# Kernel tuning notes

Hardware: AMD Instinct MI355X
Metric: run time of the kernel (lower is better)

Reference implementation:

```python
import jax, jax.numpy as jnp
import numpy as np

FACTOR = 2
GAIN = 1.0

def _setup_fir(fir=(1, 3, 3, 1), gain=GAIN):
    k = np.asarray(fir, dtype=np.float32)
    if k.ndim == 1:
        k = np.outer(k, k)
    k = k / k.sum() * gain
    return k  # (4, 4)

def setup_inputs() -> dict:
    key = jax.random.key(0)
    kx, kw = jax.random.split(key)
    N, C, H, W = 16, 320, 64, 64
    x = jax.random.normal(kx, (N, C, H, W), dtype=jnp.float32)
    # variance-scaling uniform init (DDPM style): fan_in = fan_out = C*9
    fan = C * 3 * 3
    bound = float(np.sqrt(3.0 / fan))
    w = jax.random.uniform(kw, (C, C, 3, 3), dtype=jnp.float32, minval=-bound, maxval=bound)
    fir_k = jnp.asarray(_setup_fir())
    return {"x": x, "w": w, "fir_k": fir_k}

def reference(x, w, fir_k):
    # Fused FIR (upfirdn2d with up=1, down=1) + strided 3x3 conv downsample.
    C = x.shape[1]
    convW = w.shape[3]          # 3
    kH = fir_k.shape[0]         # 4
    p = kH - FACTOR + (convW - 1)           # 4
    pad0, pad1 = (p + 1) // 2, p // 2       # (2, 2)
    # upfirdn2d: zero-pad then true convolution (flipped kernel), depthwise
    xp = jnp.pad(x, ((0, 0), (0, 0), (pad0, pad1), (pad0, pad1)))
    kf = jnp.flip(fir_k, (0, 1))            # symmetric here, kept for faithfulness
    kd = jnp.broadcast_to(kf[None, None], (C, 1, kH, kH))
    y = jax.lax.conv_general_dilated(
        xp, kd, window_strides=(1, 1), padding='VALID',
        dimension_numbers=('NCHW', 'OIHW', 'NCHW'), feature_group_count=C)
    # strided conv2d, padding=0, stride=factor
    out = jax.lax.conv_general_dilated(
        y, w, window_strides=(FACTOR, FACTOR), padding='VALID',
        dimension_numbers=('NCHW', 'OIHW', 'NCHW'))
    return out  # [N, C, H//2, W//2]
```

## Files before the change

kernel.cpp:

```cpp
#include <hip/hip_runtime.h>
#include <hip/hip_bf16.h>


typedef short bf16x8_t __attribute__((ext_vector_type(8)));
typedef float f32x4 __attribute__((ext_vector_type(4)));
typedef __attribute__((address_space(1))) const unsigned int* as1_u32p;
typedef __attribute__((address_space(3))) unsigned int* as3_u32p;

#define NI 16
#define CCH 320
#define HW 64
#define HY 65
#define HY2 4225
#define CCSTEP 135200

__global__ __launch_bounds__(256) void fir_kernel(const float* __restrict__ x,
                                                  const float* __restrict__ fir_k,
                                                  __hip_bfloat16* __restrict__ yt) {
    __shared__ float vlds[8 * 68 * 17];
    int bx = blockIdx.x;
    int n   = bx / 180;
    int rr  = bx % 180;
    int r0  = (rr / 20) * 8;
    int ci0 = (rr % 20) * 16;

    float f0 = fir_k[0] + fir_k[1] + fir_k[2] + fir_k[3];
    float f1 = fir_k[4] + fir_k[5] + fir_k[6] + fir_k[7];
    float f2 = fir_k[8] + fir_k[9] + fir_k[10] + fir_k[11];
    float f3 = fir_k[12] + fir_k[13] + fir_k[14] + fir_k[15];

    int tid = threadIdx.x;
    int lane = tid & 63;
    int g = tid >> 6;

    for (int cis = g; cis < 16; cis += 4) {
        int ci = ci0 + cis;
        const float* xb = x + (size_t)(n * CCH + ci) * HW * HW;
        float xr[11];
#pragma unroll
        for (int jr = 0; jr < 11; ++jr) {
            int row = r0 + jr - 2;
            xr[jr] = (row >= 0 && row < HW) ? xb[row * HW + lane] : 0.f;
        }
#pragma unroll
        for (int j = 0; j < 8; ++j) {
            float v = f0 * xr[j] + f1 * xr[j + 1] + f2 * xr[j + 2] + f3 * xr[j + 3];
            vlds[(j * 68 + lane + 2) * 17 + cis] = v;
            if (lane < 2)   vlds[(j * 68 + lane) * 17 + cis] = 0.f;
            if (lane >= 62) vlds[(j * 68 + lane + 4) * 17 + cis] = 0.f;
        }
    }
    __syncthreads();

    int p  = tid & 7;
    int cl = tid >> 3;
    int cis0 = 2 * p;
    int ci  = ci0 + cis0;
    size_t obase = (size_t)(n * 10 + (ci >> 5)) * HY2 * 32 + (ci & 31);
    unsigned int* ytp = (unsigned int*)yt;
#pragma unroll
    for (int j = 0; j < 8; ++j) {
        if (r0 + j >= HY) break;
#pragma unroll
        for (int cb = 0; cb < 3; ++cb) {
            int c = cb * 32 + cl;
            if (c < HY) {
                int vb = (j * 68 + c) * 17;
                float y0 = f0 * vlds[vb + cis0]      + f1 * vlds[vb + 17 + cis0]
                         + f2 * vlds[vb + 34 + cis0] + f3 * vlds[vb + 51 + cis0];
                float y1 = f0 * vlds[vb + cis0 + 1]      + f1 * vlds[vb + 17 + cis0 + 1]
                         + f2 * vlds[vb + 34 + cis0 + 1] + f3 * vlds[vb + 51 + cis0 + 1];
                unsigned int b0 = (__bfloat16_as_ushort(__float2bfloat16(y0)));
                unsigned int b1 = (__bfloat16_as_ushort(__float2bfloat16(y1)));
                ytp[(obase + (size_t)((r0 + j) * HY + c) * 32) >> 1] = b0 | (b1 << 16);
            }
        }
    }
}

__global__ __launch_bounds__(256) void wt2_kernel(const float* __restrict__ w,
                                                  __hip_bfloat16* __restrict__ wt) {
    int idx = blockIdx.x * 256 + threadIdx.x;
    if (idx < 9 * CCH * CCH) {
        int j  = idx & 7;
        int co = (idx >> 3) % CCH;
        int t2 = idx / 2560;
        int q  = t2 & 3;
        int cc = (t2 >> 2) % 10;
        int tap = t2 / 40;
        int ci = cc * 32 + q * 8 + j;
        wt[idx] = __float2bfloat16(w[(co * CCH + ci) * 9 + tap]);
    }
}

__global__ __launch_bounds__(256, 3) void conv_kernel(const __hip_bfloat16* __restrict__ yt,
                                                      const __hip_bfloat16* __restrict__ wt2,
                                                      float* __restrict__ out) {
    __shared__ short ylds[2][1536 * 8];

    int bx = blockIdx.x;
    int sp = bx & 15;
    int t  = bx >> 4;
    int cb = t % 5;
    int n  = t / 5;
    int co0 = cb * 64;
    int oh0 = (sp >> 1) * 4;
    int ow0 = (sp & 1) * 16;

    int tid = threadIdx.x;
    int lane = tid & 63;
    int wid = tid >> 6;
    int q = lane >> 4, lc = lane & 15;

    const unsigned short* ytu = (const unsigned short*)yt;
    const unsigned short* wtu = (const unsigned short*)wt2;

    int ybase = (n * 10 * HY2 + (2 * oh0) * HY + 2 * ow0) * 32;
    int goff[6];
#pragma unroll
    for (int k = 0; k < 6; ++k) {
        int u = k * 256 + tid;
        int uc = (u < 1485) ? u : 1484;
        int p = uc / 5, s = uc - p * 5;
        if (s == 4) s = 3;
        int pr = p / 33, pc = p - pr * 33;
        goff[k] = ybase + (pr * HY + pc) * 32 + s * 8;
    }

    const unsigned short* wbl = wtu + q * 2560 + (size_t)(co0 + wid * 16 + lc) * 8;
    const int aoff = (2 * lc) * 40 + q * 8;

    f32x4 acc[4];
#pragma unroll
    for (int i = 0; i < 4; ++i) acc[i] = (f32x4){0.f, 0.f, 0.f, 0.f};

    bf16x8_t bfr[2][9];

#define GLDS(buf, K, ccidx)                                                            \
    __builtin_amdgcn_global_load_lds(                                                  \
        (as1_u32p)(ytu + goff[K] + (ccidx) * CCSTEP),                                  \
        (as3_u32p)(&ylds[buf][(size_t)((K) * 256 + wid * 64) * 8]), 16, 0, 0)

#pragma unroll
    for (int k = 0; k < 6; ++k) GLDS(0, k, 0);
#pragma unroll
    for (int kk = 0; kk < 9; ++kk)
        bfr[0][kk] = *(const bf16x8_t*)(wbl + kk * 102400);
    __syncthreads();

    auto compute = [&](const short* buf, const bf16x8_t* b) {
#pragma unroll
        for (int kw = 0; kw < 3; ++kw) {
            bf16x8_t af[9];
#pragma unroll
            for (int r = 0; r < 9; ++r)
                af[r] = *(const bf16x8_t*)(buf + aoff + (r * 33 + kw) * 40);
#pragma unroll
            for (int kh = 0; kh < 3; ++kh)
#pragma unroll
                for (int mf = 0; mf < 4; ++mf)
                    acc[mf] = __builtin_amdgcn_mfma_f32_16x16x32_bf16(
                        b[kh * 3 + kw], af[2 * mf + kh], acc[mf], 0, 0, 0);
        }
    };

    for (int tt = 0; tt < 5; ++tt) {
        int cc0 = 2 * tt, cc1 = 2 * tt + 1;
        {
#pragma unroll
            for (int k = 0; k < 6; ++k) GLDS(1, k, cc0 + 1);
            const unsigned short* wnx = wbl + (cc0 + 1) * 10240;
#pragma unroll
            for (int kk = 0; kk < 9; ++kk)
                bfr[1][kk] = *(const bf16x8_t*)(wnx + kk * 102400);
            compute(&ylds[0][0], bfr[0]);
            __syncthreads();
        }
        {
            if (cc1 < 9) {
#pragma unroll
                for (int k = 0; k < 6; ++k) GLDS(0, k, cc1 + 1);
                const unsigned short* wnx = wbl + (cc1 + 1) * 10240;
#pragma unroll
                for (int kk = 0; kk < 9; ++kk)
                    bfr[0][kk] = *(const bf16x8_t*)(wnx + kk * 102400);
            }
            compute(&ylds[1][0], bfr[1]);
            if (cc1 < 9) __syncthreads();
        }
    }
#undef GLDS

#pragma unroll
    for (int mf = 0; mf < 4; ++mf) {
        int oh = oh0 + mf;
        int ow = ow0 + lc;
#pragma unroll
        for (int rg = 0; rg < 4; ++rg) {
            int co = co0 + wid * 16 + q * 4 + rg;
            out[((n * CCH + co) * 32 + oh) * 32 + ow] = acc[mf][rg];
        }
    }
}

__global__ __launch_bounds__(256) void naive_kernel(const float* __restrict__ x,
                                                    const float* __restrict__ w,
                                                    const float* __restrict__ fk,
                                                    float* __restrict__ out) {
    int idx = blockIdx.x * 256 + threadIdx.x;
    if (idx >= NI * CCH * 32 * 32) return;
    int ow = idx & 31;
    int oh = (idx >> 5) & 31;
    int co = (idx >> 10) % CCH;
    int n = (idx >> 10) / CCH;
    float f0 = fk[0] + fk[1] + fk[2] + fk[3];
    float f1 = fk[4] + fk[5] + fk[6] + fk[7];
    float f2 = fk[8] + fk[9] + fk[10] + fk[11];
    float f3 = fk[12] + fk[13] + fk[14] + fk[15];
    float fv[4] = {f0, f1, f2, f3};
    float acc = 0.f;
    for (int ci = 0; ci < CCH; ++ci) {
        const float* xb = x + (size_t)(n * CCH + ci) * HW * HW;
        const float* wb = w + (size_t)(co * CCH + ci) * 9;
#pragma unroll
        for (int u = 0; u < 3; ++u) {
            int yr = 2 * oh + u;
#pragma unroll
            for (int v = 0; v < 3; ++v) {
                int yc = 2 * ow + v;
                float s = 0.f;
#pragma unroll
                for (int a = 0; a < 4; ++a) {
                    int xrw = yr - 2 + a;
                    if (xrw < 0 || xrw >= HW) continue;
                    float t = 0.f;
#pragma unroll
                    for (int b = 0; b < 4; ++b) {
                        int xc = yc - 2 + b;
                        if (xc >= 0 && xc < HW) t += fv[b] * xb[xrw * HW + xc];
                    }
                    s += fv[a] * t;
                }
                acc += wb[u * 3 + v] * s;
            }
        }
    }
    out[idx] = acc;
}

extern "C" void kernel_launch(void* const* d_in, const int* in_sizes, int n_in,
                              void* d_out, int out_size, void* d_ws, size_t ws_size,
                              hipStream_t stream) {
    const float* x = (const float*)d_in[0];
    const float* w = (const float*)d_in[1];
    const float* fk = (const float*)d_in[2];
    float* out = (float*)d_out;

    const size_t ybytes = (size_t)NI * 10 * HY2 * 32 * 2;
    const size_t wtoff = ybytes;
    const size_t need = wtoff + (size_t)9 * CCH * CCH * 2;

    if (ws_size >= need) {
        __hip_bfloat16* yt = (__hip_bfloat16*)d_ws;
        __hip_bfloat16* wt = (__hip_bfloat16*)((char*)d_ws + wtoff);
        fir_kernel<<<16 * 9 * 20, 256, 0, stream>>>(x, fk, yt);
        wt2_kernel<<<(9 * CCH * CCH + 255) / 256, 256, 0, stream>>>(w, wt);
        conv_kernel<<<16 * 5 * 16, 256, 0, stream>>>(yt, wt, out);
    } else {
        naive_kernel<<<(NI * CCH * 32 * 32 + 255) / 256, 256, 0, stream>>>(x, w, fk, out);
    }
}
```

Before: 79.73 us.

## Switch intermediate FIR buffer to 8-channel-octet planar layout with 16-byte stores

The bf16 intermediate changes from a [n][cc][pixel][32ch] layout to [n][octet][pixel][8ch], so each pixel's 8 channels form one contiguous 16-byte chunk. The FIR kernel's LDS layout becomes per-channel rows, and each thread now writes 8 channels with a single vector store instead of scattered 4-byte stores. The conv kernel's global-to-LDS offsets are updated to the new layout. This aims to coalesce the FIR kernel's writes, but the conv loads now stride across octet planes rather than a contiguous 64-byte pixel chunk, and lane 63 does extra serial work.

```diff
diff --git a/kernel.cpp b/kernel.cpp
--- a/kernel.cpp
+++ b/kernel.cpp
@@ -4,6 +4,7 @@
 
 typedef short bf16x8_t __attribute__((ext_vector_type(8)));
 typedef float f32x4 __attribute__((ext_vector_type(4)));
+typedef unsigned int u32x4 __attribute__((ext_vector_type(4)));
 typedef __attribute__((address_space(1))) const unsigned int* as1_u32p;
 typedef __attribute__((address_space(3))) unsigned int* as3_u32p;
 
@@ -17,7 +18,7 @@
 __global__ __launch_bounds__(256) void fir_kernel(const float* __restrict__ x,
                                                   const float* __restrict__ fir_k,
                                                   __hip_bfloat16* __restrict__ yt) {
-    __shared__ float vlds[8 * 68 * 17];
+    __shared__ float vlds[8 * 16 * 69];
     int bx = blockIdx.x;
     int n   = bx / 180;
     int rr  = bx % 180;
@@ -45,35 +46,41 @@
 #pragma unroll
         for (int j = 0; j < 8; ++j) {
             float v = f0 * xr[j] + f1 * xr[j + 1] + f2 * xr[j + 2] + f3 * xr[j + 3];
-            vlds[(j * 68 + lane + 2) * 17 + cis] = v;
-            if (lane < 2)   vlds[(j * 68 + lane) * 17 + cis] = 0.f;
-            if (lane >= 62) vlds[(j * 68 + lane + 4) * 17 + cis] = 0.f;
+            float* vrow = vlds + (j * 16 + cis) * 69;
+            vrow[lane + 2] = v;
+            if (lane < 2)   vrow[lane] = 0.f;
+            if (lane >= 62) vrow[lane + 4] = 0.f;
         }
     }
     __syncthreads();
 
-    int p  = tid & 7;
-    int cl = tid >> 3;
-    int cis0 = 2 * p;
-    int ci  = ci0 + cis0;
-    size_t obase = (size_t)(n * 10 + (ci >> 5)) * HY2 * 32 + (ci & 31);
-    unsigned int* ytp = (unsigned int*)yt;
-#pragma unroll
-    for (int j = 0; j < 8; ++j) {
-        if (r0 + j >= HY) break;
-#pragma unroll
-        for (int cb = 0; cb < 3; ++cb) {
-            int c = cb * 32 + cl;
-            if (c < HY) {
-                int vb = (j * 68 + c) * 17;
-                float y0 = f0 * vlds[vb + cis0]      + f1 * vlds[vb + 17 + cis0]
-                         + f2 * vlds[vb + 34 + cis0] + f3 * vlds[vb + 51 + cis0];
-                float y1 = f0 * vlds[vb + cis0 + 1]      + f1 * vlds[vb + 17 + cis0 + 1]
-                         + f2 * vlds[vb + 34 + cis0 + 1] + f3 * vlds[vb + 51 + cis0 + 1];
-                unsigned int b0 = (__bfloat16_as_ushort(__float2bfloat16(y0)));
-                unsigned int b1 = (__bfloat16_as_ushort(__float2bfloat16(y1)));
-                ytp[(obase + (size_t)((r0 + j) * HY + c) * 32) >> 1] = b0 | (b1 << 16);
-            }
+    unsigned short* yu = (unsigned short*)yt;
+#pragma unroll
+    for (int i = 0; i < 4; ++i) {
+        int slot = 4 * i + g;
+        int j = slot >> 1, oct = slot & 1;
+        int r = r0 + j;
+        if (r >= HY) continue;
+        int qg = (rr % 20) * 2 + oct;
+        size_t obase = ((size_t)(n * 40 + qg) * HY2 + (size_t)r * HY) * 8;
+        const float* vb = vlds + (j * 16 + oct * 8) * 69;
+        int nc = (lane == 63) ? 2 : 1;
+        for (int e = 0; e < nc; ++e) {
+            int c = lane + e;
+            float a[8];
+#pragma unroll
+            for (int u = 0; u < 8; ++u) {
+                const float* vr = vb + u * 69 + c;
+                a[u] = f0 * vr[0] + f1 * vr[1] + f2 * vr[2] + f3 * vr[3];
+            }
+            unsigned int wd[4];
+#pragma unroll
+            for (int h = 0; h < 4; ++h) {
+                unsigned int lo = __bfloat16_as_ushort(__float2bfloat16(a[2 * h]));
+                unsigned int hi = __bfloat16_as_ushort(__float2bfloat16(a[2 * h + 1]));
+                wd[h] = lo | (hi << 16);
+            }
+            *(u32x4*)(yu + obase + (size_t)c * 8) = (u32x4){wd[0], wd[1], wd[2], wd[3]};
         }
     }
 }
@@ -115,7 +122,7 @@
     const unsigned short* ytu = (const unsigned short*)yt;
     const unsigned short* wtu = (const unsigned short*)wt2;
 
-    int ybase = (n * 10 * HY2 + (2 * oh0) * HY + 2 * ow0) * 32;
+    int ybase = n * 40 * HY2 * 8 + ((2 * oh0) * HY + 2 * ow0) * 8;
     int goff[6];
 #pragma unroll
     for (int k = 0; k < 6; ++k) {
@@ -124,7 +131,7 @@
         int p = uc / 5, s = uc - p * 5;
         if (s == 4) s = 3;
         int pr = p / 33, pc = p - pr * 33;
-        goff[k] = ybase + (pr * HY + pc) * 32 + s * 8;
+        goff[k] = ybase + (s * HY2 + pr * HY + pc) * 8;
     }
 
     const unsigned short* wbl = wtu + q * 2560 + (size_t)(co0 + wid * 16 + lc) * 8;
@@ -256,7 +263,7 @@
     const float* fk = (const float*)d_in[2];
     float* out = (float*)d_out;
 
-    const size_t ybytes = (size_t)NI * 10 * HY2 * 32 * 2;
+    const size_t ybytes = (size_t)NI * 40 * HY2 * 8 * 2;
     const size_t wtoff = ybytes;
     const size_t need = wtoff + (size_t)9 * CCH * CCH * 2;
 
```

Result: no change. 78.93 us (-1.0%).
